# Optimization experiments

Hardware: AMD Instinct MI355X
Metric: run time of the kernel (lower is better)

## Reference

```python
import jax, jax.numpy as jnp
import numpy as np

D = 1024      # embed_size
H = 16        # num_heads
NEXP = 8      # num_experts
TOPK = 3
THRESH = 0.05
COEF = 0.01
B, SQ, SKV = 4, 1024, 1024


def _ln(x, g, b, eps=1e-5):
    m = jnp.mean(x, axis=-1, keepdims=True)
    v = jnp.mean(jnp.square(x - m), axis=-1, keepdims=True)
    return (x - m) * jax.lax.rsqrt(v + eps) * g + b


def setup_inputs() -> dict:
    key = jax.random.key(0)
    ks = jax.random.split(key, 20)
    s = 0.02
    w = lambda k, shape: (jax.random.normal(k, shape, jnp.float32) * s)
    return {
        'query': jax.random.normal(ks[0], (B, SQ, D), jnp.float32),
        'key_value': jax.random.normal(ks[1], (B, SKV, D), jnp.float32),
        'Wq': w(ks[2], (D, D)), 'bq': jnp.zeros((D,), jnp.float32),
        'Wk': w(ks[3], (D, D)), 'bk': jnp.zeros((D,), jnp.float32),
        'Wv': w(ks[4], (D, D)), 'bv': jnp.zeros((D,), jnp.float32),
        'W_in': w(ks[5], (3 * D, D)), 'b_in': jnp.zeros((3 * D,), jnp.float32),
        'W_out': w(ks[6], (D, D)), 'b_out': jnp.zeros((D,), jnp.float32),
        'Wa': w(ks[7], (D, D)), 'ba': jnp.zeros((D,), jnp.float32),
        'ln1_g': jnp.ones((D,), jnp.float32), 'ln1_b': jnp.zeros((D,), jnp.float32),
        'Wg': w(ks[8], (D, NEXP)),
        'ew1': w(ks[9], (NEXP, D, 4 * D)), 'eb1': jnp.zeros((NEXP, 4 * D), jnp.float32),
        'ew2': w(ks[10], (NEXP, 4 * D, D)), 'eb2': jnp.zeros((NEXP, D), jnp.float32),
        'ln2_g': jnp.ones((D,), jnp.float32), 'ln2_b': jnp.zeros((D,), jnp.float32),
    }


def reference(query, key_value, Wq, bq, Wk, bk, Wv, bv, W_in, b_in, W_out, b_out,
              Wa, ba, ln1_g, ln1_b, Wg, ew1, eb1, ew2, eb2, ln2_g, ln2_b):
    Bq, Sq, _ = query.shape
    Skv = key_value.shape[1]
    Dh = D // H
    # outer Q/K/V linears (torch Linear: x @ W.T + b)
    q = query @ Wq.T + bq
    k = key_value @ Wk.T + bk
    v = key_value @ Wv.T + bv
    # nn.MultiheadAttention in-projection
    Wiq, Wik, Wiv = jnp.split(W_in, 3, axis=0)
    biq, bik, biv = jnp.split(b_in, 3)
    qh = (q @ Wiq.T + biq).reshape(Bq, Sq, H, Dh).transpose(0, 2, 1, 3)
    kh = (k @ Wik.T + bik).reshape(Bq, Skv, H, Dh).transpose(0, 2, 1, 3)
    vh = (v @ Wiv.T + biv).reshape(Bq, Skv, H, Dh).transpose(0, 2, 1, 3)
    scores = jnp.einsum('bhqd,bhkd->bhqk', qh, kh) / jnp.sqrt(jnp.float32(Dh))
    attn = jax.nn.softmax(scores, axis=-1)
    o = jnp.einsum('bhqk,bhkd->bhqd', attn, vh).transpose(0, 2, 1, 3).reshape(Bq, Sq, D)
    o = o @ W_out.T + b_out
    # adapt + residual + first_norm
    x = _ln(o @ Wa.T + ba + query, ln1_g, ln1_b)
    # ---- MoE: top-3 softmax gating, threshold on non-top-1 gates ----
    probs = jax.nn.softmax(x @ Wg, axis=-1)                 # [B,S,E]
    topv, topi = jax.lax.top_k(probs, TOPK)                  # [B,S,3]
    keep = jnp.concatenate([jnp.ones_like(topv[..., :1], bool),
                            topv[..., 1:] >= THRESH], axis=-1)
    topv = jnp.where(keep, topv, 0.0)
    combine = jnp.sum(jax.nn.one_hot(topi, NEXP, dtype=x.dtype) * topv[..., None], axis=-2)  # [B,S,E]
    moe_out = jnp.zeros_like(x)
    for e in range(NEXP):  # small fixed expert count
        h = jax.nn.gelu(x @ ew1[e] + eb1[e], approximate=False)
        moe_out = moe_out + combine[..., e:e + 1] * (h @ ew2[e] + eb2[e])
    # load-balance aux loss: E * sum(frac_routed * mean_prob) * coef
    fe = jnp.mean((combine > 0).astype(x.dtype), axis=(0, 1))
    me = jnp.mean(probs, axis=(0, 1))
    aux = COEF * NEXP * jnp.sum(fe * me)
    out = _ln(moe_out + x, ln2_g, ln2_b)
    return out, aux
```

## Files before the change

### kernel.cpp

```cpp
#include <hip/hip_runtime.h>
#include <math.h>

#define THRESH_C 0.05f
#define COEF_C   0.01f

typedef __bf16 bf16;
typedef __bf16 bf16x8 __attribute__((ext_vector_type(8)));
typedef __bf16 bf16x4 __attribute__((ext_vector_type(4)));
typedef float  f32x4  __attribute__((ext_vector_type(4)));

__device__ __forceinline__ void ld16(void* lds_base, const void* g) {
    __builtin_amdgcn_global_load_lds(
        (const __attribute__((address_space(1))) void*)g,
        (__attribute__((address_space(3))) void*)lds_base,
        16, 0, 0);
}

__global__ __launch_bounds__(256) void k_f32_to_split(const float* __restrict__ in,
                                                      bf16* __restrict__ hi,
                                                      bf16* __restrict__ lo, long n) {
    long i = ((long)blockIdx.x * 256 + threadIdx.x) * 4;
    if (i >= n) return;
    float4 v = *(const float4*)(in + i);
    bf16x4 h, l;
    h[0] = (bf16)v.x; l[0] = (bf16)(v.x - (float)h[0]);
    h[1] = (bf16)v.y; l[1] = (bf16)(v.y - (float)h[1]);
    h[2] = (bf16)v.z; l[2] = (bf16)(v.z - (float)h[2]);
    h[3] = (bf16)v.w; l[3] = (bf16)(v.w - (float)h[3]);
    *(bf16x4*)(hi + i) = h;
    *(bf16x4*)(lo + i) = l;
}

__global__ __launch_bounds__(256) void k_transpose4_split(const float* __restrict__ w0,
                                                          const float* __restrict__ w1,
                                                          const float* __restrict__ w2,
                                                          const float* __restrict__ w3,
                                                          bf16* __restrict__ oh,
                                                          bf16* __restrict__ ol) {
    __shared__ float t[64][65];
    int z = blockIdx.z;
    const float* in = (z == 0) ? w0 : (z == 1) ? w1 : (z == 2) ? w2 : w3;
    bf16* ohz = oh + (long)z * 1048576;
    bf16* olz = ol + (long)z * 1048576;
    int r0 = blockIdx.y * 64, c0 = blockIdx.x * 64;
    for (int i = threadIdx.x; i < 4096; i += 256) {
        int r = i >> 6, c = i & 63;
        t[r][c] = in[(long)(r0 + r) * 1024 + (c0 + c)];
    }
    __syncthreads();
    for (int i = threadIdx.x; i < 4096; i += 256) {
        int c = i >> 6, r = i & 63;
        float v = t[r][c];
        bf16 h = (bf16)v;
        long o = (long)(c0 + c) * 1024 + (r0 + r);
        ohz[o] = h;
        olz[o] = (bf16)(v - (float)h);
    }
}

__global__ __launch_bounds__(256) void k_transpose_ew(const float* __restrict__ in,
                                                      bf16* __restrict__ out,
                                                      int R, int C) {
    __shared__ bf16 t[64][65];
    const float* ib = in + (long)blockIdx.z * R * C;
    bf16* ob = out + (long)blockIdx.z * R * C;
    int r0 = blockIdx.y * 64, c0 = blockIdx.x * 64;
    for (int i = threadIdx.x; i < 4096; i += 256) {
        int r = i >> 6, c = i & 63;
        t[r][c] = (bf16)ib[(long)(r0 + r) * C + (c0 + c)];
    }
    __syncthreads();
    for (int i = threadIdx.x; i < 4096; i += 256) {
        int c = i >> 6, r = i & 63;
        ob[(long)(c0 + c) * R + (r0 + r)] = t[r][c];
    }
}

__global__ __launch_bounds__(256) void k_bias_fold4(const float* __restrict__ W_in,
                                                    const float* __restrict__ Wa,
                                                    const float* __restrict__ bq,
                                                    const float* __restrict__ bk,
                                                    const float* __restrict__ bv,
                                                    const float* __restrict__ b_out,
                                                    const float* __restrict__ b_in,
                                                    const float* __restrict__ ba,
                                                    float* __restrict__ y) {
    int z = blockIdx.y;
    const float* W  = (z < 3) ? (W_in + (long)z * 1048576) : Wa;
    const float* b1 = (z == 0) ? bq : (z == 1) ? bk : (z == 2) ? bv : b_out;
    const float* b2 = (z < 3) ? (b_in + z * 1024) : ba;
    int row = blockIdx.x * 4 + (threadIdx.x >> 6);
    int lane = threadIdx.x & 63;
    const float* wr = W + (long)row * 1024;
    float s = 0.f;
    for (int k = lane; k < 1024; k += 64) s += wr[k] * b1[k];
#pragma unroll
    for (int o = 32; o >= 1; o >>= 1) s += __shfl_xor(s, o);
    if (lane == 0) y[z * 1024 + row] = b2[row] + s;
}

enum { HP_SPLIT = 0, HP_F32 = 1, HP_SPLIT_HEADS = 2 };

template<int MODE>
__global__ __launch_bounds__(256)
void gemm_hp(const bf16* __restrict__ Ah, const bf16* __restrict__ Al, int lda, long sAz,
             const bf16* __restrict__ Bh, const bf16* __restrict__ Bl, int ldb, long sBz,
             void* __restrict__ Chv, bf16* __restrict__ Cl, int ldc, long sCz,
             const float* __restrict__ bias, float alpha, int M, int N, int K) {
    __shared__ alignas(16) bf16 sAh[128 * 32];
    __shared__ alignas(16) bf16 sAl[128 * 32];
    __shared__ alignas(16) bf16 sBh[128 * 32];
    __shared__ alignas(16) bf16 sBl[128 * 32];
    const int bm = blockIdx.y, bn = blockIdx.x, z = blockIdx.z;
    const int tid  = threadIdx.x;
    const int lane = tid & 63, wave = tid >> 6;
    const int quad = lane >> 4, l16 = lane & 15;
    const int wr = wave >> 1, wc = wave & 1;
    const int sr = tid >> 2;
    const int sc = (tid & 3) * 8;

    int arow0 = min(bm * 128 + sr, M - 1);
    int arow1 = min(bm * 128 + sr + 64, M - 1);
    int brow0 = min(bn * 128 + sr, N - 1);
    int brow1 = min(bn * 128 + sr + 64, N - 1);

    const bf16* pAh0 = Ah + (long)z * sAz + (long)arow0 * lda + sc;
    const bf16* pAh1 = Ah + (long)z * sAz + (long)arow1 * lda + sc;
    const bf16* pAl0 = Al + (long)z * sAz + (long)arow0 * lda + sc;
    const bf16* pAl1 = Al + (long)z * sAz + (long)arow1 * lda + sc;
    const bf16* pBh0 = Bh + (long)z * sBz + (long)brow0 * ldb + sc;
    const bf16* pBh1 = Bh + (long)z * sBz + (long)brow1 * ldb + sc;
    const bf16* pBl0 = Bl + (long)z * sBz + (long)brow0 * ldb + sc;
    const bf16* pBl1 = Bl + (long)z * sBz + (long)brow1 * ldb + sc;
    const int wo = wave << 9;

    f32x4 acc[4][4];
#pragma unroll
    for (int i = 0; i < 4; i++)
#pragma unroll
        for (int j = 0; j < 4; j++) acc[i][j] = (f32x4){0.f, 0.f, 0.f, 0.f};

    for (int k0 = 0; k0 < K; k0 += 32) {
        __syncthreads();
        ld16(sAh + wo,        pAh0 + k0);
        ld16(sAh + 2048 + wo, pAh1 + k0);
        ld16(sAl + wo,        pAl0 + k0);
        ld16(sAl + 2048 + wo, pAl1 + k0);
        ld16(sBh + wo,        pBh0 + k0);
        ld16(sBh + 2048 + wo, pBh1 + k0);
        ld16(sBl + wo,        pBl0 + k0);
        ld16(sBl + 2048 + wo, pBl1 + k0);
        __syncthreads();
        bf16x8 ah[4], al[4], bh[4], bl[4];
#pragma unroll
        for (int i = 0; i < 4; i++) {
            int ro = (wr * 64 + i * 16 + l16) * 32 + quad * 8;
            ah[i] = *(const bf16x8*)&sAh[ro];
            al[i] = *(const bf16x8*)&sAl[ro];
        }
#pragma unroll
        for (int j = 0; j < 4; j++) {
            int ro = (wc * 64 + j * 16 + l16) * 32 + quad * 8;
            bh[j] = *(const bf16x8*)&sBh[ro];
            bl[j] = *(const bf16x8*)&sBl[ro];
        }
#pragma unroll
        for (int i = 0; i < 4; i++)
#pragma unroll
            for (int j = 0; j < 4; j++) {
                acc[i][j] = __builtin_amdgcn_mfma_f32_16x16x32_bf16(al[i], bh[j], acc[i][j], 0, 0, 0);
                acc[i][j] = __builtin_amdgcn_mfma_f32_16x16x32_bf16(ah[i], bl[j], acc[i][j], 0, 0, 0);
                acc[i][j] = __builtin_amdgcn_mfma_f32_16x16x32_bf16(ah[i], bh[j], acc[i][j], 0, 0, 0);
            }
    }

#pragma unroll
    for (int i = 0; i < 4; i++) {
        int mbase = bm * 128 + wr * 64 + i * 16 + quad * 4;
#pragma unroll
        for (int j = 0; j < 4; j++) {
            int n = bn * 128 + wc * 64 + j * 16 + l16;
            if (n < N) {
                float bv = bias ? bias[n] : 0.f;
#pragma unroll
                for (int r = 0; r < 4; r++) {
                    int m = mbase + r;
                    if (m < M) {
                        float v = alpha * acc[i][j][r] + bv;
                        if (MODE == HP_SPLIT) {
                            long cidx = (long)z * sCz + (long)m * ldc + n;
                            bf16 h = (bf16)v;
                            ((bf16*)Chv)[cidx] = h;
                            Cl[cidx] = (bf16)(v - (float)h);
                        } else if (MODE == HP_F32) {
                            long cidx = (long)z * sCz + (long)m * ldc + n;
                            ((float*)Chv)[cidx] = v;
                        } else {
                            int slice = ((m >> 10) << 4) + (n >> 6);
                            long idx = (long)slice * 65536 + (long)(m & 1023) * 64 + (n & 63);
                            bf16 h = (bf16)v;
                            ((bf16*)Chv)[idx] = h;
                            Cl[idx] = (bf16)(v - (float)h);
                        }
                    }
                }
            }
        }
    }
}

__global__ __launch_bounds__(256)
void gemm_pv(const bf16* __restrict__ Ph, const bf16* __restrict__ Pl,
             const bf16* __restrict__ Vh, const bf16* __restrict__ Vl,
             bf16* __restrict__ Oh, bf16* __restrict__ Ol) {
    __shared__ alignas(16) bf16 sAh[128 * 32];
    __shared__ alignas(16) bf16 sAl[128 * 32];
    __shared__ alignas(16) bf16 sBh[64 * 32];
    __shared__ alignas(16) bf16 sBl[64 * 32];
    const int bm = blockIdx.x, z = blockIdx.y;
    const int tid = threadIdx.x, lane = tid & 63, wave = tid >> 6;
    const int quad = lane >> 4, l16 = lane & 15;
    const int wr = wave & 1, wc = wave >> 1;
    const int sr = tid >> 2, sc = (tid & 3) * 8;

    const bf16* pA0h = Ph + (long)z * 1048576 + (long)(bm * 128 + sr) * 1024 + sc;
    const bf16* pA1h = pA0h + 64 * 1024;
    const bf16* pA0l = Pl + (long)z * 1048576 + (long)(bm * 128 + sr) * 1024 + sc;
    const bf16* pA1l = pA0l + 64 * 1024;
    const bf16* pB0h = Vh + (long)z * 65536 + (long)sr * 1024 + sc;
    const bf16* pB0l = Vl + (long)z * 65536 + (long)sr * 1024 + sc;
    const int wo = wave << 9;

    f32x4 acc[4][2];
#pragma unroll
    for (int i = 0; i < 4; i++)
#pragma unroll
        for (int j = 0; j < 2; j++) acc[i][j] = (f32x4){0.f, 0.f, 0.f, 0.f};

    for (int k0 = 0; k0 < 1024; k0 += 32) {
        __syncthreads();
        ld16(sAh + wo,        pA0h + k0);
        ld16(sAh + 2048 + wo, pA1h + k0);
        ld16(sAl + wo,        pA0l + k0);
        ld16(sAl + 2048 + wo, pA1l + k0);
        ld16(sBh + wo, pB0h + k0);
        ld16(sBl + wo, pB0l + k0);
        __syncthreads();
        bf16x8 ah[4], al[4], bh[2], bl[2];
#pragma unroll
        for (int i = 0; i < 4; i++) {
            int ro = (wr * 64 + i * 16 + l16) * 32 + quad * 8;
            ah[i] = *(const bf16x8*)&sAh[ro];
            al[i] = *(const bf16x8*)&sAl[ro];
        }
#pragma unroll
        for (int j = 0; j < 2; j++) {
            int ro = (wc * 32 + j * 16 + l16) * 32 + quad * 8;
            bh[j] = *(const bf16x8*)&sBh[ro];
            bl[j] = *(const bf16x8*)&sBl[ro];
        }
#pragma unroll
        for (int i = 0; i < 4; i++)
#pragma unroll
            for (int j = 0; j < 2; j++) {
                acc[i][j] = __builtin_amdgcn_mfma_f32_16x16x32_bf16(al[i], bh[j], acc[i][j], 0, 0, 0);
                acc[i][j] = __builtin_amdgcn_mfma_f32_16x16x32_bf16(ah[i], bl[j], acc[i][j], 0, 0, 0);
                acc[i][j] = __builtin_amdgcn_mfma_f32_16x16x32_bf16(ah[i], bh[j], acc[i][j], 0, 0, 0);
            }
    }

#pragma unroll
    for (int i = 0; i < 4; i++) {
        int mbase = bm * 128 + wr * 64 + i * 16 + quad * 4;
#pragma unroll
        for (int j = 0; j < 2; j++) {
            int n = wc * 32 + j * 16 + l16;
#pragma unroll
            for (int r = 0; r < 4; r++) {
                int m = mbase + r;
                long idx = (long)z * 65536 + (long)m * 64 + n;
                float v = acc[i][j][r];
                bf16 h = (bf16)v;
                Oh[idx] = h;
                Ol[idx] = (bf16)(v - (float)h);
            }
        }
    }
}

__global__ __launch_bounds__(256)
void gemm_moe1(const bf16* __restrict__ Ae, const bf16* __restrict__ ew1t,
               const float* __restrict__ eb1, bf16* __restrict__ Hp,
               const int* __restrict__ counts, const int* __restrict__ bases) {
    const int e = blockIdx.z;
    const int M = counts[e];
    const int bm = blockIdx.y, bn = blockIdx.x;
    if (bm * 128 >= M) return;
    const bf16* A = Ae + (long)bases[e] * 1024;
    const bf16* B = ew1t + (long)e * 4194304;
    bf16* C = Hp + (long)bases[e] * 4096;
    const float* bias = eb1 + e * 4096;

    __shared__ alignas(16) bf16 sA[128 * 32];
    __shared__ alignas(16) bf16 sB[128 * 32];
    const int tid  = threadIdx.x;
    const int lane = tid & 63, wave = tid >> 6;
    const int quad = lane >> 4, l16 = lane & 15;
    const int wr = wave >> 1, wc = wave & 1;
    const int sr = tid >> 2;
    const int sc = (tid & 3) * 8;

    int arow0 = min(bm * 128 + sr, M - 1);
    int arow1 = min(bm * 128 + sr + 64, M - 1);
    int brow0 = bn * 128 + sr;
    const bf16* pA0 = A + (long)arow0 * 1024 + sc;
    const bf16* pA1 = A + (long)arow1 * 1024 + sc;
    const bf16* pB0 = B + (long)brow0 * 1024 + sc;
    const bf16* pB1 = B + (long)(brow0 + 64) * 1024 + sc;
    const int wo = wave << 9;

    f32x4 acc[4][4];
#pragma unroll
    for (int i = 0; i < 4; i++)
#pragma unroll
        for (int j = 0; j < 4; j++) acc[i][j] = (f32x4){0.f, 0.f, 0.f, 0.f};

    for (int k0 = 0; k0 < 1024; k0 += 32) {
        __syncthreads();
        ld16(sA + wo,        pA0 + k0);
        ld16(sA + 2048 + wo, pA1 + k0);
        ld16(sB + wo,        pB0 + k0);
        ld16(sB + 2048 + wo, pB1 + k0);
        __syncthreads();
        bf16x8 af[4], bfr[4];
#pragma unroll
        for (int i = 0; i < 4; i++)
            af[i] = *(const bf16x8*)&sA[(wr * 64 + i * 16 + l16) * 32 + quad * 8];
#pragma unroll
        for (int j = 0; j < 4; j++)
            bfr[j] = *(const bf16x8*)&sB[(wc * 64 + j * 16 + l16) * 32 + quad * 8];
#pragma unroll
        for (int i = 0; i < 4; i++)
#pragma unroll
            for (int j = 0; j < 4; j++)
                acc[i][j] = __builtin_amdgcn_mfma_f32_16x16x32_bf16(af[i], bfr[j], acc[i][j], 0, 0, 0);
    }

#pragma unroll
    for (int i = 0; i < 4; i++) {
        int mbase = bm * 128 + wr * 64 + i * 16 + quad * 4;
#pragma unroll
        for (int j = 0; j < 4; j++) {
            int n = bn * 128 + wc * 64 + j * 16 + l16;
            float bv = bias[n];
#pragma unroll
            for (int r = 0; r < 4; r++) {
                int m = mbase + r;
                if (m < M) {
                    float v = acc[i][j][r] + bv;
                    float g = 0.5f * v * (1.f + erff(v * 0.70710678118654752f));
                    C[(long)m * 4096 + n] = (bf16)g;
                }
            }
        }
    }
}

__global__ __launch_bounds__(256)
void gemm_moe2(const bf16* __restrict__ Hp, const bf16* __restrict__ ew2t,
               float* __restrict__ Y,
               const int* __restrict__ counts, const int* __restrict__ bases) {
    const int e = blockIdx.z;
    const int M = counts[e];
    const int bm = blockIdx.y;
    const int bn = blockIdx.x;
    if (bm * 128 >= M) return;
    const bf16* A = Hp + (long)bases[e] * 4096;
    const bf16* B = ew2t + (long)e * 4194304;
    float* C = Y + (long)bases[e] * 1024;

    __shared__ alignas(16) bf16 sA[128 * 32];
    __shared__ alignas(16) bf16 sB[128 * 32];
    const int tid  = threadIdx.x;
    const int lane = tid & 63, wave = tid >> 6;
    const int quad = lane >> 4, l16 = lane & 15;
    const int wr = wave >> 1, wc = wave & 1;
    const int sr = tid >> 2;
    const int sc = (tid & 3) * 8;

    int arow0 = min(bm * 128 + sr, M - 1);
    int arow1 = min(bm * 128 + sr + 64, M - 1);
    int brow0 = bn * 128 + sr;
    const bf16* pA0 = A + (long)arow0 * 4096 + sc;
    const bf16* pA1 = A + (long)arow1 * 4096 + sc;
    const bf16* pB0 = B + (long)brow0 * 4096 + sc;
    const bf16* pB1 = B + (long)(brow0 + 64) * 4096 + sc;
    const int wo = wave << 9;

    f32x4 acc[4][4];
#pragma unroll
    for (int i = 0; i < 4; i++)
#pragma unroll
        for (int j = 0; j < 4; j++) acc[i][j] = (f32x4){0.f, 0.f, 0.f, 0.f};

    for (int k0 = 0; k0 < 4096; k0 += 32) {
        __syncthreads();
        ld16(sA + wo,        pA0 + k0);
        ld16(sA + 2048 + wo, pA1 + k0);
        ld16(sB + wo,        pB0 + k0);
        ld16(sB + 2048 + wo, pB1 + k0);
        __syncthreads();
        bf16x8 af[4], bfr[4];
#pragma unroll
        for (int i = 0; i < 4; i++)
            af[i] = *(const bf16x8*)&sA[(wr * 64 + i * 16 + l16) * 32 + quad * 8];
#pragma unroll
        for (int j = 0; j < 4; j++)
            bfr[j] = *(const bf16x8*)&sB[(wc * 64 + j * 16 + l16) * 32 + quad * 8];
#pragma unroll
        for (int i = 0; i < 4; i++)
#pragma unroll
            for (int j = 0; j < 4; j++)
                acc[i][j] = __builtin_amdgcn_mfma_f32_16x16x32_bf16(af[i], bfr[j], acc[i][j], 0, 0, 0);
    }

#pragma unroll
    for (int i = 0; i < 4; i++) {
        int mbase = bm * 128 + wr * 64 + i * 16 + quad * 4;
#pragma unroll
        for (int j = 0; j < 4; j++) {
            int n = bn * 128 + wc * 64 + j * 16 + l16;
#pragma unroll
            for (int r = 0; r < 4; r++) {
                int m = mbase + r;
                if (m < M) C[(long)m * 1024 + n] = acc[i][j][r];
            }
        }
    }
}

__global__ __launch_bounds__(256) void k_vsplit(const bf16* __restrict__ VH_h,
                                                const bf16* __restrict__ VH_l,
                                                bf16* __restrict__ VT_h,
                                                bf16* __restrict__ VT_l) {
    __shared__ bf16 th[64][65];
    __shared__ bf16 tl[64][65];
    int s = blockIdx.y, q0 = blockIdx.x * 64;
    int b = s >> 4, h = s & 15;
    long ibase = ((long)(b * 1024 + q0)) * 1024 + h * 64;
    for (int i = threadIdx.x; i < 4096; i += 256) {
        int q = i >> 6, d = i & 63;
        th[q][d] = VH_h[ibase + (long)q * 1024 + d];
        tl[q][d] = VH_l[ibase + (long)q * 1024 + d];
    }
    __syncthreads();
    long obase = (long)s * 65536 + q0;
    for (int i = threadIdx.x; i < 4096; i += 256) {
        int d = i >> 6, q = i & 63;
        VT_h[obase + (long)d * 1024 + q] = th[q][d];
        VT_l[obase + (long)d * 1024 + q] = tl[q][d];
    }
}

__global__ __launch_bounds__(256) void k_ocopy(const bf16* __restrict__ Op_h,
                                               const bf16* __restrict__ Op_l,
                                               bf16* __restrict__ O_h,
                                               bf16* __restrict__ O_l) {
    int t = blockIdx.x * 4 + (threadIdx.x >> 6);
    int lane = threadIdx.x & 63;
    int b = t >> 10, q = t & 1023;
    int h = lane >> 2, dd = (lane & 3) * 16;
    long src = ((long)(b * 16 + h)) * 65536 + (long)q * 64 + dd;
    long dst = (long)t * 1024 + h * 64 + dd;
    *(bf16x8*)(O_h + dst)     = *(const bf16x8*)(Op_h + src);
    *(bf16x8*)(O_h + dst + 8) = *(const bf16x8*)(Op_h + src + 8);
    *(bf16x8*)(O_l + dst)     = *(const bf16x8*)(Op_l + src);
    *(bf16x8*)(O_l + dst + 8) = *(const bf16x8*)(Op_l + src + 8);
}

__global__ __launch_bounds__(256) void k_gather(const bf16* __restrict__ Xb,
                                                const int* __restrict__ tok,
                                                const int* __restrict__ counts,
                                                const int* __restrict__ bases,
                                                bf16* __restrict__ Ae) {
    int e = blockIdx.y;
    int cnt = counts[e];
    long base = bases[e];
    for (int i = blockIdx.x; i < cnt; i += gridDim.x) {
        int t = tok[e * 4096 + i];
        const bf16x4* src = (const bf16x4*)(Xb + (long)t * 1024);
        bf16x4* dst = (bf16x4*)(Ae + (base + i) * 1024);
        dst[threadIdx.x] = src[threadIdx.x];
    }
}

__global__ __launch_bounds__(256) void k_softmax_ip(bf16* __restrict__ Sh,
                                                    bf16* __restrict__ Sl) {
    int row = blockIdx.x * 4 + (threadIdx.x >> 6);
    int lane = threadIdx.x & 63;
    long o = (long)row * 1024 + lane * 16;
    bf16x8 h0 = *(const bf16x8*)(Sh + o), h1 = *(const bf16x8*)(Sh + o + 8);
    bf16x8 l0 = *(const bf16x8*)(Sl + o), l1 = *(const bf16x8*)(Sl + o + 8);
    float v[16];
#pragma unroll
    for (int i = 0; i < 8; i++) {
        v[i] = (float)h0[i] + (float)l0[i];
        v[8 + i] = (float)h1[i] + (float)l1[i];
    }
    float mx = v[0];
#pragma unroll
    for (int i = 1; i < 16; i++) mx = fmaxf(mx, v[i]);
#pragma unroll
    for (int of = 32; of >= 1; of >>= 1) mx = fmaxf(mx, __shfl_xor(mx, of));
    float s = 0.f;
#pragma unroll
    for (int i = 0; i < 16; i++) { v[i] = expf(v[i] - mx); s += v[i]; }
#pragma unroll
    for (int of = 32; of >= 1; of >>= 1) s += __shfl_xor(s, of);
    float inv = 1.f / s;
#pragma unroll
    for (int i = 0; i < 8; i++) {
        float a = v[i] * inv;
        h0[i] = (bf16)a; l0[i] = (bf16)(a - (float)h0[i]);
        float b = v[8 + i] * inv;
        h1[i] = (bf16)b; l1[i] = (bf16)(b - (float)h1[i]);
    }
    *(bf16x8*)(Sh + o) = h0;  *(bf16x8*)(Sh + o + 8) = h1;
    *(bf16x8*)(Sl + o) = l0;  *(bf16x8*)(Sl + o + 8) = l1;
}

__global__ __launch_bounds__(256) void k_ln(const float* __restrict__ xin,
                                            const float* __restrict__ resid,
                                            const float* __restrict__ g,
                                            const float* __restrict__ bb,
                                            float* __restrict__ outf,
                                            bf16* __restrict__ outb) {
    int row = blockIdx.x * 4 + (threadIdx.x >> 6);
    int lane = threadIdx.x & 63;
    long base = (long)row * 1024 + lane * 16;
    float v[16];
#pragma unroll
    for (int i = 0; i < 16; i += 4) {
        f32x4 a = *(const f32x4*)(xin + base + i);
        if (resid) { f32x4 r4 = *(const f32x4*)(resid + base + i); a += r4; }
        v[i] = a[0]; v[i + 1] = a[1]; v[i + 2] = a[2]; v[i + 3] = a[3];
    }
    float s = 0.f;
#pragma unroll
    for (int i = 0; i < 16; i++) s += v[i];
#pragma unroll
    for (int o = 32; o >= 1; o >>= 1) s += __shfl_xor(s, o);
    float mean = s * (1.f / 1024.f);
    float vs = 0.f;
#pragma unroll
    for (int i = 0; i < 16; i++) { float d = v[i] - mean; vs += d * d; }
#pragma unroll
    for (int o = 32; o >= 1; o >>= 1) vs += __shfl_xor(vs, o);
    float inv = 1.f / sqrtf(vs * (1.f / 1024.f) + 1e-5f);
    const float* gp = g + lane * 16;
    const float* bp = bb + lane * 16;
#pragma unroll
    for (int i = 0; i < 16; i++) {
        float o = (v[i] - mean) * inv * gp[i] + bp[i];
        if (outf) outf[base + i] = o;
        if (outb) outb[base + i] = (bf16)o;
    }
}

__global__ __launch_bounds__(256) void k_moe_ln(const float* __restrict__ Y,
                                                const int* __restrict__ pos,
                                                const float* __restrict__ combine,
                                                const float* __restrict__ eb2,
                                                const float* __restrict__ resid,
                                                const float* __restrict__ g,
                                                const float* __restrict__ bb,
                                                float* __restrict__ outf) {
    int row = blockIdx.x * 4 + (threadIdx.x >> 6);
    int lane = threadIdx.x & 63;
    long base = (long)row * 1024 + lane * 16;
    float v[16];
#pragma unroll
    for (int i = 0; i < 16; i += 4) {
        f32x4 a = *(const f32x4*)(resid + base + i);
        v[i] = a[0]; v[i + 1] = a[1]; v[i + 2] = a[2]; v[i + 3] = a[3];
    }
    for (int e = 0; e < 8; e++) {
        int p = pos[row * 8 + e];
        if (p >= 0) {
            float c = combine[row * 8 + e];
            const float* yr = Y + (long)p * 1024 + lane * 16;
            const float* br = eb2 + e * 1024 + lane * 16;
#pragma unroll
            for (int i = 0; i < 16; i += 4) {
                f32x4 y4 = *(const f32x4*)(yr + i);
                f32x4 b4 = *(const f32x4*)(br + i);
                v[i]     += c * (y4[0] + b4[0]);
                v[i + 1] += c * (y4[1] + b4[1]);
                v[i + 2] += c * (y4[2] + b4[2]);
                v[i + 3] += c * (y4[3] + b4[3]);
            }
        }
    }
    float s = 0.f;
#pragma unroll
    for (int i = 0; i < 16; i++) s += v[i];
#pragma unroll
    for (int o = 32; o >= 1; o >>= 1) s += __shfl_xor(s, o);
    float mean = s * (1.f / 1024.f);
    float vs = 0.f;
#pragma unroll
    for (int i = 0; i < 16; i++) { float d = v[i] - mean; vs += d * d; }
#pragma unroll
    for (int o = 32; o >= 1; o >>= 1) vs += __shfl_xor(vs, o);
    float inv = 1.f / sqrtf(vs * (1.f / 1024.f) + 1e-5f);
    const float* gp = g + lane * 16;
    const float* bp = bb + lane * 16;
#pragma unroll
    for (int i = 0; i < 16; i++)
        outf[base + i] = (v[i] - mean) * inv * gp[i] + bp[i];
}

__global__ __launch_bounds__(256) void k_gate(const float* __restrict__ X,
                                              const float* __restrict__ Wg,
                                              float* __restrict__ combine,
                                              float* __restrict__ partials) {
    __shared__ float sm[16];
    if (threadIdx.x < 16) sm[threadIdx.x] = 0.f;
    __syncthreads();
    int t = blockIdx.x * 4 + (threadIdx.x >> 6);
    int lane = threadIdx.x & 63;
    const float* x = X + (long)t * 1024;
    float acc[8] = {0.f, 0.f, 0.f, 0.f, 0.f, 0.f, 0.f, 0.f};
    for (int i = lane; i < 1024; i += 64) {
        float xv = x[i];
        const float* w = Wg + i * 8;
#pragma unroll
        for (int e = 0; e < 8; e++) acc[e] += xv * w[e];
    }
#pragma unroll
    for (int e = 0; e < 8; e++)
#pragma unroll
        for (int o = 32; o >= 1; o >>= 1) acc[e] += __shfl_xor(acc[e], o);
    if (lane == 0) {
        float mx = acc[0];
#pragma unroll
        for (int e = 1; e < 8; e++) mx = fmaxf(mx, acc[e]);
        float p[8], s = 0.f;
#pragma unroll
        for (int e = 0; e < 8; e++) { p[e] = expf(acc[e] - mx); s += p[e]; }
        float invs = 1.f / s;
#pragma unroll
        for (int e = 0; e < 8; e++) p[e] *= invs;
        float b1 = -1.f, b2 = -1.f, b3 = -1.f; int i1 = 0, i2 = 0, i3 = 0;
#pragma unroll
        for (int e = 0; e < 8; e++) {
            float pe = p[e];
            if (pe > b1)      { b3 = b2; i3 = i2; b2 = b1; i2 = i1; b1 = pe; i1 = e; }
            else if (pe > b2) { b3 = b2; i3 = i2; b2 = pe; i2 = e; }
            else if (pe > b3) { b3 = pe; i3 = e; }
        }
        float c[8] = {0.f, 0.f, 0.f, 0.f, 0.f, 0.f, 0.f, 0.f};
        c[i1] = b1;
        if (b2 >= THRESH_C) c[i2] = b2;
        if (b3 >= THRESH_C) c[i3] = b3;
        float* co = combine + (long)t * 8;
#pragma unroll
        for (int e = 0; e < 8; e++) co[e] = c[e];
#pragma unroll
        for (int e = 0; e < 8; e++) {
            atomicAdd(&sm[e], p[e]);
            if (c[e] > 0.f) atomicAdd(&sm[8 + e], 1.f);
        }
    }
    __syncthreads();
    if (threadIdx.x < 16) partials[(long)blockIdx.x * 16 + threadIdx.x] = sm[threadIdx.x];
}

__global__ __launch_bounds__(256) void k_route(const float* __restrict__ combine,
                                               int* __restrict__ counts,
                                               int* __restrict__ bases,
                                               int* __restrict__ tok,
                                               int* __restrict__ pos) {
    __shared__ int scan[256];
    int tid = threadIdx.x;
    int mybase = 0;
    for (int e = 0; e < 8; e++) {
        int pred[16]; int cnt = 0;
#pragma unroll
        for (int j = 0; j < 16; j++) {
            int t = tid * 16 + j;
            pred[j] = combine[t * 8 + e] > 0.f ? 1 : 0;
            cnt += pred[j];
        }
        scan[tid] = cnt;
        __syncthreads();
        for (int off = 1; off < 256; off <<= 1) {
            int v = (tid >= off) ? scan[tid - off] : 0;
            __syncthreads();
            scan[tid] += v;
            __syncthreads();
        }
        int start = scan[tid] - cnt;
        int total = scan[255];
        int o = e * 4096 + start;
        int gp = mybase + start;
#pragma unroll
        for (int j = 0; j < 16; j++) {
            int t = tid * 16 + j;
            if (pred[j]) { tok[o++] = t; pos[t * 8 + e] = gp++; }
            else pos[t * 8 + e] = -1;
        }
        if (tid == 0) { counts[e] = total; bases[e] = mybase; }
        mybase += total;
        __syncthreads();
    }
}

__global__ __launch_bounds__(256) void k_aux(const float* __restrict__ partials, int nblocks,
                                             float* __restrict__ auxout) {
    __shared__ float red[256];
    int tid = threadIdx.x;
    int e = tid & 15, grp = tid >> 4;
    float s = 0.f;
    for (int b = grp; b < nblocks; b += 16) s += partials[(long)b * 16 + e];
    red[tid] = s;
    __syncthreads();
    if (grp == 0) {
        float tot = 0.f;
        for (int g2 = 0; g2 < 16; g2++) tot += red[g2 * 16 + e];
        red[tid] = tot;
    }
    __syncthreads();
    if (tid == 0) {
        float s2 = 0.f;
        for (int e2 = 0; e2 < 8; e2++)
            s2 += (red[8 + e2] * (1.f / 4096.f)) * (red[e2] * (1.f / 4096.f));
        auxout[0] = COEF_C * 8.f * s2;
    }
}

extern "C" void kernel_launch(void* const* d_in, const int* in_sizes, int n_in,
                              void* d_out, int out_size, void* d_ws, size_t ws_size,
                              hipStream_t stream) {
    const float* query     = (const float*)d_in[0];
    const float* key_value = (const float*)d_in[1];
    const float* Wq   = (const float*)d_in[2];
    const float* bq   = (const float*)d_in[3];
    const float* Wk   = (const float*)d_in[4];
    const float* bk   = (const float*)d_in[5];
    const float* Wv   = (const float*)d_in[6];
    const float* bv   = (const float*)d_in[7];
    const float* W_in = (const float*)d_in[8];
    const float* b_in = (const float*)d_in[9];
    const float* W_out = (const float*)d_in[10];
    const float* b_out = (const float*)d_in[11];
    const float* Wa   = (const float*)d_in[12];
    const float* ba   = (const float*)d_in[13];
    const float* ln1_g = (const float*)d_in[14];
    const float* ln1_b = (const float*)d_in[15];
    const float* Wg   = (const float*)d_in[16];
    const float* ew1  = (const float*)d_in[17];
    const float* eb1  = (const float*)d_in[18];
    const float* ew2  = (const float*)d_in[19];
    const float* eb2  = (const float*)d_in[20];
    const float* ln2_g = (const float*)d_in[21];
    const float* ln2_b = (const float*)d_in[22];

    const size_t MBY = 1ull << 20;
    const long MB1 = 1024L * 1024L;
    char* ws = (char*)d_ws;

    bf16* Sh   = (bf16*)(ws + 0 * MBY);
    bf16* Sl   = (bf16*)(ws + 64 * MBY);
    bf16* ew1t = (bf16*)(ws + 0 * MBY);
    bf16* ew2t = (bf16*)(ws + 64 * MBY);
    bf16* WAll_h = (bf16*)(ws + 128 * MBY);
    bf16* WAll_l = (bf16*)(ws + 136 * MBY);
    bf16* WT_h   = (bf16*)(ws + 144 * MBY);
    bf16* WT_l   = (bf16*)(ws + 152 * MBY);
    bf16* Xq_h  = (bf16*)(ws + 160 * MBY), *Xq_l  = (bf16*)(ws + 168 * MBY);
    bf16* Xkv_h = (bf16*)(ws + 176 * MBY), *Xkv_l = (bf16*)(ws + 184 * MBY);
    bf16* O_h  = (bf16*)(ws + 160 * MBY), *O_l  = (bf16*)(ws + 168 * MBY);
    bf16* QHp_h = (bf16*)(ws + 192 * MBY), *QHp_l = (bf16*)(ws + 200 * MBY);
    bf16* KHp_h = (bf16*)(ws + 208 * MBY), *KHp_l = (bf16*)(ws + 216 * MBY);
    bf16* VH_h  = (bf16*)(ws + 224 * MBY), *VH_l  = (bf16*)(ws + 232 * MBY);
    bf16* VTp_h = (bf16*)(ws + 240 * MBY), *VTp_l = (bf16*)(ws + 248 * MBY);
    bf16* Op_h  = (bf16*)(ws + 256 * MBY), *Op_l  = (bf16*)(ws + 264 * MBY);
    float* Xf   = (float*)(ws + 256 * MBY);
    float* Af   = (float*)(ws + 272 * MBY);
    bf16* Ae      = (bf16*)(ws + 128 * MBY);
    bf16* Hp      = (bf16*)(ws + 152 * MBY);
    float* Yp     = (float*)(ws + 272 * MBY);
    bf16* Xb   = (bf16*)(ws + 320 * MBY);
    bf16* Weff_h = (bf16*)(ws + 328 * MBY);
    bf16* Weff_l = (bf16*)(ws + 336 * MBY);
    float* combine  = (float*)(ws + 344 * MBY);
    float* partials = (float*)(ws + 344 * MBY + 128 * 1024);
    float* beff     = (float*)(ws + 344 * MBY + 192 * 1024);
    int*   counts   = (int*)  (ws + 344 * MBY + 212 * 1024);
    int*   bases    = (int*)  (ws + 344 * MBY + 213 * 1024);
    int*   tok      = (int*)  (ws + 344 * MBY + 214 * 1024);
    int*   pos      = (int*)  (ws + 344 * MBY + 342 * 1024);

    dim3 blk(256);

    k_f32_to_split<<<4096, blk, 0, stream>>>(query, Xq_h, Xq_l, 4L * MB1);
    k_f32_to_split<<<4096, blk, 0, stream>>>(key_value, Xkv_h, Xkv_l, 4L * MB1);
    k_f32_to_split<<<3072, blk, 0, stream>>>(W_in, WAll_h, WAll_l, 3L * MB1);
    k_f32_to_split<<<1024, blk, 0, stream>>>(Wa, WAll_h + 3 * MB1, WAll_l + 3 * MB1, MB1);
    k_transpose4_split<<<dim3(16, 16, 4), blk, 0, stream>>>(Wq, Wk, Wv, W_out, WT_h, WT_l);
    k_bias_fold4<<<dim3(256, 4), blk, 0, stream>>>(W_in, Wa, bq, bk, bv, b_out, b_in, ba, beff);

    gemm_hp<HP_SPLIT><<<dim3(8, 8, 4), blk, 0, stream>>>(
        WAll_h, WAll_l, 1024, MB1, WT_h, WT_l, 1024, MB1,
        Weff_h, Weff_l, 1024, MB1, nullptr, 1.f, 1024, 1024, 1024);

    dim3 gP(8, 32, 1);
    gemm_hp<HP_SPLIT_HEADS><<<gP, blk, 0, stream>>>(Xq_h, Xq_l, 1024, 0, Weff_h, Weff_l, 1024, 0,
                                                    QHp_h, QHp_l, 0, 0, beff, 1.f, 4096, 1024, 1024);
    gemm_hp<HP_SPLIT_HEADS><<<gP, blk, 0, stream>>>(Xkv_h, Xkv_l, 1024, 0, Weff_h + MB1, Weff_l + MB1, 1024, 0,
                                                    KHp_h, KHp_l, 0, 0, beff + 1024, 1.f, 4096, 1024, 1024);
    gemm_hp<HP_SPLIT><<<gP, blk, 0, stream>>>(Xkv_h, Xkv_l, 1024, 0, Weff_h + 2 * MB1, Weff_l + 2 * MB1, 1024, 0,
                                              VH_h, VH_l, 1024, 0, beff + 2048, 1.f, 4096, 1024, 1024);
    k_vsplit<<<dim3(16, 64), blk, 0, stream>>>(VH_h, VH_l, VTp_h, VTp_l);

    for (int half = 0; half < 2; half++) {
        long so = (long)half * 32 * 65536;
        gemm_hp<HP_SPLIT><<<dim3(8, 8, 32), blk, 0, stream>>>(
            QHp_h + so, QHp_l + so, 64, 65536,
            KHp_h + so, KHp_l + so, 64, 65536,
            Sh, Sl, 1024, MB1, nullptr, 0.125f, 1024, 1024, 64);
        k_softmax_ip<<<8192, blk, 0, stream>>>(Sh, Sl);
        gemm_pv<<<dim3(8, 32), blk, 0, stream>>>(Sh, Sl, VTp_h + so, VTp_l + so,
                                                 Op_h + so, Op_l + so);
    }
    k_ocopy<<<1024, blk, 0, stream>>>(Op_h, Op_l, O_h, O_l);

    gemm_hp<HP_F32><<<gP, blk, 0, stream>>>(O_h, O_l, 1024, 0, Weff_h + 3 * MB1, Weff_l + 3 * MB1, 1024, 0,
                                            Af, nullptr, 1024, 0, beff + 3072, 1.f, 4096, 1024, 1024);
    k_ln<<<1024, blk, 0, stream>>>(Af, query, ln1_g, ln1_b, Xf, Xb);
    k_gate<<<1024, blk, 0, stream>>>(Xf, Wg, combine, partials);
    k_route<<<1, blk, 0, stream>>>(combine, counts, bases, tok, pos);
    k_gather<<<dim3(512, 8), blk, 0, stream>>>(Xb, tok, counts, bases, Ae);

    k_transpose_ew<<<dim3(64, 16, 8), blk, 0, stream>>>(ew1, ew1t, 1024, 4096);
    k_transpose_ew<<<dim3(16, 64, 8), blk, 0, stream>>>(ew2, ew2t, 4096, 1024);

    gemm_moe1<<<dim3(32, 32, 8), blk, 0, stream>>>(Ae, ew1t, eb1, Hp, counts, bases);
    gemm_moe2<<<dim3(8, 32, 8), blk, 0, stream>>>(Hp, ew2t, Yp, counts, bases);

    k_moe_ln<<<1024, blk, 0, stream>>>(Yp, pos, combine, eb2, Xf, ln2_g, ln2_b, (float*)d_out);
    k_aux<<<1, blk, 0, stream>>>(partials, 1024, (float*)d_out + (out_size - 1));
}
```

Before: 1.603 ms.

## Compact MoE GEMM grids with routed tile list and XCD-aware block swizzle

The routing kernel now writes a compact list of (expert, row-tile) pairs and its length, and both MoE GEMMs launch a 1D grid sized to the maximum possible tile count (104). Each block reads its tile from that list instead of indexing a dense 32x32x8 grid where most blocks exit early. Block IDs are also remapped so that consecutive logical blocks, which share expert weight tiles, land on the same XCD for better L2 reuse. This removes the launch and scheduling cost of empty blocks, but depends on the 104-tile bound being large enough and adds a serial tile-list loop on one thread in k_route.

```diff
diff --git a/kernel.cpp b/kernel.cpp
--- a/kernel.cpp
+++ b/kernel.cpp
@@ -14,6 +14,12 @@
         (const __attribute__((address_space(1))) void*)g,
         (__attribute__((address_space(3))) void*)lds_base,
         16, 0, 0);
+}
+
+__device__ __forceinline__ int xcd_swz(int orig, int nwg) {
+    int q = nwg >> 3, r = nwg & 7;
+    int xcd = orig & 7, idx = orig >> 3;
+    return (xcd < r ? xcd * (q + 1) : r * (q + 1) + (xcd - r) * q) + idx;
 }
 
 __global__ __launch_bounds__(256) void k_f32_to_split(const float* __restrict__ in,
@@ -291,11 +297,15 @@
 __global__ __launch_bounds__(256)
 void gemm_moe1(const bf16* __restrict__ Ae, const bf16* __restrict__ ew1t,
                const float* __restrict__ eb1, bf16* __restrict__ Hp,
-               const int* __restrict__ counts, const int* __restrict__ bases) {
-    const int e = blockIdx.z;
+               const int* __restrict__ counts, const int* __restrict__ bases,
+               const int* __restrict__ tiles, const int* __restrict__ ntile) {
+    const int wg = xcd_swz(blockIdx.x, gridDim.x);
+    const int tile = wg >> 5;
+    const int bn = wg & 31;
+    if (tile >= ntile[0]) return;
+    const int te = tiles[tile];
+    const int e = te >> 16, bm = te & 0xffff;
     const int M = counts[e];
-    const int bm = blockIdx.y, bn = blockIdx.x;
-    if (bm * 128 >= M) return;
     const bf16* A = Ae + (long)bases[e] * 1024;
     const bf16* B = ew1t + (long)e * 4194304;
     bf16* C = Hp + (long)bases[e] * 4096;
@@ -369,12 +379,15 @@
 __global__ __launch_bounds__(256)
 void gemm_moe2(const bf16* __restrict__ Hp, const bf16* __restrict__ ew2t,
                float* __restrict__ Y,
-               const int* __restrict__ counts, const int* __restrict__ bases) {
-    const int e = blockIdx.z;
+               const int* __restrict__ counts, const int* __restrict__ bases,
+               const int* __restrict__ tiles, const int* __restrict__ ntile) {
+    const int wg = xcd_swz(blockIdx.x, gridDim.x);
+    const int tile = wg >> 3;
+    const int bn = wg & 7;
+    if (tile >= ntile[0]) return;
+    const int te = tiles[tile];
+    const int e = te >> 16, bm = te & 0xffff;
     const int M = counts[e];
-    const int bm = blockIdx.y;
-    const int bn = blockIdx.x;
-    if (bm * 128 >= M) return;
     const bf16* A = Hp + (long)bases[e] * 4096;
     const bf16* B = ew2t + (long)e * 4194304;
     float* C = Y + (long)bases[e] * 1024;
@@ -680,10 +693,13 @@
                                                int* __restrict__ counts,
                                                int* __restrict__ bases,
                                                int* __restrict__ tok,
-                                               int* __restrict__ pos) {
+                                               int* __restrict__ pos,
+                                               int* __restrict__ tiles,
+                                               int* __restrict__ ntile) {
     __shared__ int scan[256];
     int tid = threadIdx.x;
     int mybase = 0;
+    int nt = 0;
     for (int e = 0; e < 8; e++) {
         int pred[16]; int cnt = 0;
 #pragma unroll
@@ -710,10 +726,15 @@
             if (pred[j]) { tok[o++] = t; pos[t * 8 + e] = gp++; }
             else pos[t * 8 + e] = -1;
         }
-        if (tid == 0) { counts[e] = total; bases[e] = mybase; }
+        if (tid == 0) {
+            counts[e] = total; bases[e] = mybase;
+            int nte = (total + 127) >> 7;
+            for (int b = 0; b < nte; b++) tiles[nt++] = (e << 16) | b;
+        }
         mybase += total;
         __syncthreads();
     }
+    if (tid == 0) ntile[0] = nt;
 }
 
 __global__ __launch_bounds__(256) void k_aux(const float* __restrict__ partials, int nblocks,
@@ -801,6 +822,8 @@
     int*   bases    = (int*)  (ws + 344 * MBY + 213 * 1024);
     int*   tok      = (int*)  (ws + 344 * MBY + 214 * 1024);
     int*   pos      = (int*)  (ws + 344 * MBY + 342 * 1024);
+    int*   tiles    = (int*)  (ws + 344 * MBY + 472 * 1024);
+    int*   ntile    = tiles + 128;
 
     dim3 blk(256);
 
@@ -840,14 +863,14 @@
                                             Af, nullptr, 1024, 0, beff + 3072, 1.f, 4096, 1024, 1024);
     k_ln<<<1024, blk, 0, stream>>>(Af, query, ln1_g, ln1_b, Xf, Xb);
     k_gate<<<1024, blk, 0, stream>>>(Xf, Wg, combine, partials);
-    k_route<<<1, blk, 0, stream>>>(combine, counts, bases, tok, pos);
+    k_route<<<1, blk, 0, stream>>>(combine, counts, bases, tok, pos, tiles, ntile);
     k_gather<<<dim3(512, 8), blk, 0, stream>>>(Xb, tok, counts, bases, Ae);
 
     k_transpose_ew<<<dim3(64, 16, 8), blk, 0, stream>>>(ew1, ew1t, 1024, 4096);
     k_transpose_ew<<<dim3(16, 64, 8), blk, 0, stream>>>(ew2, ew2t, 4096, 1024);
 
-    gemm_moe1<<<dim3(32, 32, 8), blk, 0, stream>>>(Ae, ew1t, eb1, Hp, counts, bases);
-    gemm_moe2<<<dim3(8, 32, 8), blk, 0, stream>>>(Hp, ew2t, Yp, counts, bases);
+    gemm_moe1<<<dim3(104 * 32), blk, 0, stream>>>(Ae, ew1t, eb1, Hp, counts, bases, tiles, ntile);
+    gemm_moe2<<<dim3(104 * 8), blk, 0, stream>>>(Hp, ew2t, Yp, counts, bases, tiles, ntile);
 
     k_moe_ln<<<1024, blk, 0, stream>>>(Yp, pos, combine, eb2, Xf, ln2_g, ln2_b, (float*)d_out);
     k_aux<<<1, blk, 0, stream>>>(partials, 1024, (float*)d_out + (out_size - 1));
```

Result: no change. 1.608 ms (+0.3%).
